# Performance work log

Measured on AMD Instinct MI355X. Metric: run time of the kernel, lower is better.

Reference implementation:

```python
import jax, jax.numpy as jnp
import numpy as np

V = 32000      # vocab_size
CTX = 1024     # context_length
D = 768        # n_embd
H = 12         # n_heads
HD = D // H    # head_dim
L = 6          # n_layers
DFF = 4 * D
B, S = 2, 1024
EPS = 1e-5


def _layernorm(x, w, b):
    mu = jnp.mean(x, axis=-1, keepdims=True)
    var = jnp.mean(jnp.square(x - mu), axis=-1, keepdims=True)
    return (x - mu) * jax.lax.rsqrt(var + EPS) * w + b


def setup_inputs() -> dict:
    key = jax.random.key(0)
    ks = iter(jax.random.split(key, 32))
    s = 0.02
    idx = jax.random.randint(next(ks), (B, S), 0, V)
    p = {
        "idx": idx,
        "tok_emb": jax.random.normal(next(ks), (V, D), jnp.float32) * s,
        "pos_emb": jax.random.normal(next(ks), (CTX, D), jnp.float32) * s,
        "ln1_w": jnp.ones((L, D)), "ln1_b": jnp.zeros((L, D)),
        "Wq": jax.random.normal(next(ks), (L, D, D), jnp.float32) * s,
        "bq": jnp.zeros((L, D)),
        "Wk": jax.random.normal(next(ks), (L, D, D), jnp.float32) * s,
        "bk": jnp.zeros((L, D)),
        "Wv": jax.random.normal(next(ks), (L, D, D), jnp.float32) * s,
        "bv": jnp.zeros((L, D)),
        "Wo": jax.random.normal(next(ks), (L, D, D), jnp.float32) * s,
        "bo": jnp.zeros((L, D)),
        "ln2_w": jnp.ones((L, D)), "ln2_b": jnp.zeros((L, D)),
        "W1": jax.random.normal(next(ks), (L, D, DFF), jnp.float32) * s,
        "b1": jnp.zeros((L, DFF)),
        "W2": jax.random.normal(next(ks), (L, DFF, D), jnp.float32) * s,
        "b2": jnp.zeros((L, D)),
        "lnf_w": jnp.ones((D,)), "lnf_b": jnp.zeros((D,)),
        "lm_head_w": jax.random.normal(next(ks), (D, V), jnp.float32) * s,
    }
    return p


def _forward(idx, tok_emb, pos_emb, ln1_w, ln1_b, Wq, bq, Wk, bk, Wv, bv,
             Wo, bo, ln2_w, ln2_b, W1, b1, W2, b2, lnf_w, lnf_b, lm_head_w):
    b, s = idx.shape
    x = tok_emb[idx] + pos_emb[:s]  # [B,S,D]
    mask = jnp.tril(jnp.ones((s, s), dtype=bool))  # causal
    scale = 1.0 / np.sqrt(HD)
    for l in range(L):
        # --- attention ---
        h = _layernorm(x, ln1_w[l], ln1_b[l])
        q = (h @ Wq[l] + bq[l]).reshape(b, s, H, HD).transpose(0, 2, 1, 3)
        k = (h @ Wk[l] + bk[l]).reshape(b, s, H, HD).transpose(0, 2, 1, 3)
        v = (h @ Wv[l] + bv[l]).reshape(b, s, H, HD).transpose(0, 2, 1, 3)
        att = jnp.einsum('bhqd,bhkd->bhqk', q, k) * scale
        att = jnp.where(mask, att, -jnp.inf)
        att = jax.nn.softmax(att, axis=-1)
        y = jnp.einsum('bhqk,bhkd->bhqd', att, v)
        y = y.transpose(0, 2, 1, 3).reshape(b, s, D)
        x = x + y @ Wo[l] + bo[l]
        # --- MLP ---
        h2 = _layernorm(x, ln2_w[l], ln2_b[l])
        x = x + jax.nn.relu(h2 @ W1[l] + b1[l]) @ W2[l] + b2[l]
    logits = _layernorm(x, lnf_w, lnf_b) @ lm_head_w  # [B,S,V]
    return logits


def reference(idx, tok_emb, pos_emb, ln1_w, ln1_b, Wq, bq, Wk, bk, Wv, bv,
              Wo, bo, ln2_w, ln2_b, W1, b1, W2, b2, lnf_w, lnf_b, lm_head_w):
    return _forward(idx, tok_emb, pos_emb, ln1_w, ln1_b, Wq, bq, Wk, bk, Wv,
                    bv, Wo, bo, ln2_w, ln2_b, W1, b1, W2, b2, lnf_w, lnf_b,
                    lm_head_w)
```

## Files before the change

### kernel.cpp

```cpp
#include <hip/hip_runtime.h>
#include <hip/hip_bf16.h>
#include <math.h>

#define D 768
#define NH 12
#define HD 64
#define NL 6
#define DFF 3072
#define BB 2
#define SS 1024
#define NROWS (BB*SS)
#define VOCAB 32000
#define QKVN (3*D)
#define LN_EPS 1e-5f

typedef __attribute__((ext_vector_type(8))) short bf16x8;
typedef __attribute__((ext_vector_type(4))) float f32x4;

typedef __attribute__((address_space(1))) const unsigned char* gas_ptr;
typedef __attribute__((address_space(3))) unsigned char* las_ptr;

__device__ __forceinline__ void load_lds16(const void* g, void* l) {
    __builtin_amdgcn_global_load_lds((gas_ptr)g, (las_ptr)l, 16, 0, 0);
}

__device__ __forceinline__ void storeOut(float* p, float v) { *p = v; }
__device__ __forceinline__ void storeOut(__hip_bfloat16* p, float v) { *p = __float2bfloat16(v); }
__device__ __forceinline__ ushort f2bs(float f) {
    __hip_bfloat16 h = __float2bfloat16(f);
    return *(ushort*)&h;
}

#define WAIT_VMCNT(n) asm volatile("s_waitcnt vmcnt(" #n ")" ::: "memory")

__global__ void embed_kernel(const int* __restrict__ idx, const float* __restrict__ tok,
                             const float* __restrict__ pos, float* __restrict__ x) {
    int row = blockIdx.x;
    int s = row % SS;
    int t = idx[row];
    for (int c = threadIdx.x; c < D; c += blockDim.x)
        x[row*D + c] = tok[(size_t)t*D + c] + pos[s*D + c];
}

template<typename OT>
__global__ __launch_bounds__(256) void layernorm_kernel(const float* __restrict__ x,
                                                        const float* __restrict__ w,
                                                        const float* __restrict__ b,
                                                        OT* __restrict__ out) {
    int row = blockIdx.x;
    __shared__ float l1[4], l2[4];
    int base = row * D;
    float vals[3];
    float s1 = 0.f, s2 = 0.f;
#pragma unroll
    for (int i = 0; i < 3; i++) {
        float v = x[base + threadIdx.x + i*256];
        vals[i] = v; s1 += v; s2 += v*v;
    }
#pragma unroll
    for (int o = 32; o > 0; o >>= 1) {
        s1 += __shfl_down(s1, o, 64);
        s2 += __shfl_down(s2, o, 64);
    }
    if ((threadIdx.x & 63) == 0) { l1[threadIdx.x >> 6] = s1; l2[threadIdx.x >> 6] = s2; }
    __syncthreads();
    float sum   = l1[0] + l1[1] + l1[2] + l1[3];
    float sumsq = l2[0] + l2[1] + l2[2] + l2[3];
    float mu  = sum * (1.f / D);
    float var = sumsq * (1.f / D) - mu * mu;
    float inv = rsqrtf(var + LN_EPS);
#pragma unroll
    for (int i = 0; i < 3; i++) {
        int c = threadIdx.x + i*256;
        storeOut(&out[base + c], (vals[i] - mu) * inv * w[c] + b[c]);
    }
}

__global__ __launch_bounds__(256) void transpose_cvt(const float* __restrict__ src,
                                                     __hip_bfloat16* __restrict__ dst,
                                                     int K, int N,
                                                     size_t srcLayerStride, size_t dstLayerStride,
                                                     int dstRowOff) {
    int l = blockIdx.z;
    src += (size_t)l * srcLayerStride;
    dst += (size_t)l * dstLayerStride + (size_t)dstRowOff * K;
    __shared__ float t[32][33];
    int k0 = blockIdx.x*32, n0 = blockIdx.y*32;
    int tx = threadIdx.x & 31, ty = threadIdx.x >> 5;
    for (int i = ty; i < 32; i += 8) t[i][tx] = src[(size_t)(k0+i)*N + n0+tx];
    __syncthreads();
    for (int i = ty; i < 32; i += 8) dst[(size_t)(n0+i)*K + k0+tx] = __float2bfloat16(t[tx][i]);
}

__global__ __launch_bounds__(256) void qkvo_trans(const float* __restrict__ Wq,
                                                  const float* __restrict__ Wk,
                                                  const float* __restrict__ Wv,
                                                  const float* __restrict__ Wo,
                                                  __hip_bfloat16* __restrict__ qkvT,
                                                  __hip_bfloat16* __restrict__ WoT) {
    int z = blockIdx.z, l = z >> 2, m = z & 3;
    const float* src = (m==0 ? Wq : m==1 ? Wk : m==2 ? Wv : Wo) + (size_t)l*D*D;
    __hip_bfloat16* dst = (m < 3) ? qkvT + (size_t)l*QKVN*D + (size_t)m*D*D
                                  : WoT  + (size_t)l*D*D;
    __shared__ float t[32][33];
    int k0 = blockIdx.x*32, n0 = blockIdx.y*32;
    int tx = threadIdx.x & 31, ty = threadIdx.x >> 5;
    for (int i = ty; i < 32; i += 8) t[i][tx] = src[(size_t)(k0+i)*D + n0+tx];
    __syncthreads();
    for (int i = ty; i < 32; i += 8) dst[(size_t)(n0+i)*D + k0+tx] = __float2bfloat16(t[tx][i]);
}

__global__ void pack_qkv_bias(const float* __restrict__ bq, const float* __restrict__ bk,
                              const float* __restrict__ bv, float* __restrict__ dst) {
    int l = blockIdx.y;
    int i = blockIdx.x*256 + threadIdx.x;
    dst[l*QKVN + i]         = bq[l*D + i];
    dst[l*QKVN + D + i]     = bk[l*D + i];
    dst[l*QKVN + 2*D + i]   = bv[l*D + i];
}

#define RG_STAGE(slot, k0) do {                                                  \
    _Pragma("unroll")                                                            \
    for (int i_ = 0; i_ < 2; i_++)                                               \
        load_lds16(A + (size_t)(bm + i_*64 + srow)*K + (k0) + sc_,               \
                   &AsR[slot][i_*64 + wid*16][0]);                               \
    load_lds16(BT + (size_t)(bn + srow)*K + (k0) + sc_,                          \
               &BsR[slot][wid*16][0]);                                           \
    } while (0)

template<typename OT, int RELU, int HASB, int VSTORE>
__global__ __launch_bounds__(256) void rg_gemm(const ushort* __restrict__ A,
                                               const ushort* __restrict__ BT,
                                               const float* __restrict__ bias,
                                               OT* __restrict__ C,
                                               ushort* __restrict__ vt,
                                               int N, int K, int gx) {
    constexpr int BM = 128, BN = 64;
    __shared__ ushort AsR[4][BM][32];
    __shared__ ushort BsR[4][BN][32];

    int id = blockIdx.x;
    int swz = (id & 7) * (gridDim.x >> 3) + (id >> 3);
    int by = swz / gx, bx = swz - by * gx;
    int bm = by * BM, bn = bx * BN;

    int tid = threadIdx.x;
    int lane = tid & 63, wid = tid >> 6;
    int wr = wid >> 1, wc = wid & 1;
    int srow = tid >> 2;
    int sc_ = ((tid & 3) ^ ((tid >> 3) & 3)) * 8;
    int fr = lane & 15, fc = lane >> 4;
    int rchunk = (fc ^ ((fr >> 1) & 3)) * 8;

    f32x4 acc[4][2];
#pragma unroll
    for (int i = 0; i < 4; i++)
#pragma unroll
        for (int j = 0; j < 2; j++)
#pragma unroll
            for (int r = 0; r < 4; r++) acc[i][j][r] = 0.f;

    const int NT = K / 32;
    RG_STAGE(0, 0);
    RG_STAGE(1, 32);
    RG_STAGE(2, 64);

    for (int t = 0; t < NT; t++) {
        int rem = NT - 1 - t;
        if (rem >= 2)      WAIT_VMCNT(6);
        else if (rem == 1) WAIT_VMCNT(3);
        else               WAIT_VMCNT(0);
        __builtin_amdgcn_s_barrier();
        asm volatile("" ::: "memory");
        if (t + 3 < NT) RG_STAGE((t+3) & 3, (t+3)*32);
        int s = t & 3;
        bf16x8 af[4], bf[2];
#pragma unroll
        for (int mi = 0; mi < 4; mi++)
            af[mi] = *(const bf16x8*)&AsR[s][wr*64 + mi*16 + fr][rchunk];
#pragma unroll
        for (int ni = 0; ni < 2; ni++)
            bf[ni] = *(const bf16x8*)&BsR[s][wc*32 + ni*16 + fr][rchunk];
        __builtin_amdgcn_s_setprio(1);
#pragma unroll
        for (int mi = 0; mi < 4; mi++)
#pragma unroll
            for (int ni = 0; ni < 2; ni++)
                acc[mi][ni] = __builtin_amdgcn_mfma_f32_16x16x32_bf16(af[mi], bf[ni], acc[mi][ni], 0, 0, 0);
        __builtin_amdgcn_s_setprio(0);
    }

    if (VSTORE && bn >= 2*D) {
        int hh = (bn - 2*D) / HD;
        int b  = bm >> 10;
        size_t vbase = ((size_t)(b*NH + hh)) * HD;
        int srow0 = (bm & (SS-1)) + wr*64 + fc*4;
#pragma unroll
        for (int mi = 0; mi < 4; mi++) {
#pragma unroll
            for (int ni = 0; ni < 2; ni++) {
                int col = bn + wc*32 + ni*16 + fr;
                int d   = wc*32 + ni*16 + fr;
                float bv_ = bias[col];
                ushort4 u;
                u.x = f2bs(acc[mi][ni][0] + bv_);
                u.y = f2bs(acc[mi][ni][1] + bv_);
                u.z = f2bs(acc[mi][ni][2] + bv_);
                u.w = f2bs(acc[mi][ni][3] + bv_);
                *(ushort4*)&vt[(vbase + d)*SS + srow0 + mi*16] = u;
            }
        }
    } else {
#pragma unroll
        for (int mi = 0; mi < 4; mi++) {
#pragma unroll
            for (int r = 0; r < 4; r++) {
                int row = bm + wr*64 + mi*16 + fc*4 + r;
#pragma unroll
                for (int ni = 0; ni < 2; ni++) {
                    int col = bn + wc*32 + ni*16 + fr;
                    float v = acc[mi][ni][r];
                    if (HASB) v += bias[col];
                    if (RELU) v = fmaxf(v, 0.f);
                    storeOut(&C[(size_t)row * N + col], v);
                }
            }
        }
    }
}

#define RSTAGE(slot, k0) do {                                                    \
    int row_ = tid >> 2;                                                         \
    load_lds16(A  + (size_t)(bm + row_)*K + (k0) + sc_,                          \
               (char*)As + (size_t)(slot)*4096 + (size_t)wid*1024);              \
    load_lds16(BT + (size_t)(bn + row_)*K + (k0) + sc_,                          \
               (char*)Bs + (size_t)(slot)*4096 + (size_t)wid*1024);              \
    } while (0)

template<int RELU>
__global__ __launch_bounds__(256) void gemm_ring64(const ushort* __restrict__ A,
                                                   const ushort* __restrict__ BT,
                                                   const float* __restrict__ bias,
                                                   const float* __restrict__ X,
                                                   float* __restrict__ C,
                                                   int N, int K, int gx) {
    __shared__ ushort As[6][64][32];
    __shared__ ushort Bs[6][64][32];

    int id = blockIdx.x;
    int swz = (id & 7) * (gridDim.x >> 3) + (id >> 3);
    int by = swz / gx, bx = swz - by * gx;
    int bm = by * 64, bn = bx * 64;

    int tid = threadIdx.x;
    int lane = tid & 63, wid = tid >> 6;
    int wr = wid >> 1, wc = wid & 1;
    int sc_ = ((lane & 3) ^ ((lane >> 3) & 3)) * 8;
    int fr = lane & 15, fc = lane >> 4;
    int rchunk = (fc ^ ((fr >> 1) & 3)) * 8;

    f32x4 acc[2][2];
#pragma unroll
    for (int i = 0; i < 2; i++)
#pragma unroll
        for (int j = 0; j < 2; j++)
#pragma unroll
            for (int r = 0; r < 4; r++) acc[i][j][r] = 0.f;

    const int NT = K / 32;
    RSTAGE(0, 0);
    RSTAGE(1, 32);
    RSTAGE(2, 64);
    RSTAGE(3, 96);
    RSTAGE(4, 128);

    for (int t = 0; t < NT; t++) {
        int rem = NT - t;
        if (rem >= 5)      WAIT_VMCNT(8);
        else if (rem == 4) WAIT_VMCNT(6);
        else if (rem == 3) WAIT_VMCNT(4);
        else if (rem == 2) WAIT_VMCNT(2);
        else               WAIT_VMCNT(0);
        __builtin_amdgcn_s_barrier();
        asm volatile("" ::: "memory");
        if (t + 5 < NT) RSTAGE((t+5) % 6, (t+5)*32);
        int s = t % 6;
        bf16x8 af[2], bf[2];
#pragma unroll
        for (int mi = 0; mi < 2; mi++)
            af[mi] = *(const bf16x8*)&As[s][wr*32 + mi*16 + fr][rchunk];
#pragma unroll
        for (int ni = 0; ni < 2; ni++)
            bf[ni] = *(const bf16x8*)&Bs[s][wc*32 + ni*16 + fr][rchunk];
        __builtin_amdgcn_s_setprio(1);
#pragma unroll
        for (int mi = 0; mi < 2; mi++)
#pragma unroll
            for (int ni = 0; ni < 2; ni++)
                acc[mi][ni] = __builtin_amdgcn_mfma_f32_16x16x32_bf16(af[mi], bf[ni], acc[mi][ni], 0, 0, 0);
        __builtin_amdgcn_s_setprio(0);
    }

#pragma unroll
    for (int mi = 0; mi < 2; mi++) {
#pragma unroll
        for (int r = 0; r < 4; r++) {
            int row = bm + wr*32 + mi*16 + fc*4 + r;
#pragma unroll
            for (int ni = 0; ni < 2; ni++) {
                int col = bn + wc*32 + ni*16 + fr;
                float v = acc[mi][ni][r] + bias[col] + X[(size_t)row * N + col];
                if (RELU) v = fmaxf(v, 0.f);
                C[(size_t)row * N + col] = v;
            }
        }
    }
}

#define LMSA3(slot, k0) do {                                                      \
    _Pragma("unroll")                                                             \
    for (int i_ = 0; i_ < 2; i_++) {                                              \
        int row_ = i_*128 + (tid >> 2);                                           \
        load_lds16(A + (size_t)(bm + row_)*D + (k0) + sc_,                        \
                   (char*)As3 + (size_t)(slot)*16384 + (size_t)(i_*512 + wid*64)*16); \
    } } while (0)
#define LMSB3(slot, k0) do {                                                      \
    _Pragma("unroll")                                                             \
    for (int i_ = 0; i_ < 2; i_++) {                                              \
        int row_ = i_*128 + (tid >> 2);                                           \
        load_lds16(BT + (size_t)(bm_n + row_)*D + (k0) + sc_,                     \
                   (char*)Bs3 + (size_t)(slot)*16384 + (size_t)(i_*512 + wid*64)*16); \
    } } while (0)

__global__ __launch_bounds__(512) void lm256_gemm(const ushort* __restrict__ A,
                                                  const ushort* __restrict__ BT,
                                                  float* __restrict__ C) {
    constexpr int NKT = D / 32;
    __shared__ ushort As3[3][256][32];
    __shared__ ushort Bs3[3][256][32];

    int id = blockIdx.x;
    int swz = (id & 7) * 125 + (id >> 3);
    int by = swz & 7;
    int bx = swz >> 3;
    int bm = by * 256, bm_n = bx * 256;

    int tid = threadIdx.x;
    int lane = tid & 63, wid = tid >> 6;
    int wr = wid >> 2, wc = wid & 3;
    int sc_ = ((tid & 3) ^ ((tid >> 3) & 3)) * 8;
    int fr = lane & 15, fc = lane >> 4;
    int rch = (fc ^ ((fr >> 1) & 3)) * 8;

    f32x4 acc[8][4];
#pragma unroll
    for (int i = 0; i < 8; i++)
#pragma unroll
        for (int j = 0; j < 4; j++)
#pragma unroll
            for (int r = 0; r < 4; r++) acc[i][j][r] = 0.f;

    LMSA3(0, 0);  LMSB3(0, 0);
    LMSA3(1, 32); LMSB3(1, 32);
    WAIT_VMCNT(4);
    __builtin_amdgcn_s_barrier();

    int s = 0;
    for (int j = 0; j < NKT; j++) {
        int s2 = s + 2; if (s2 >= 3) s2 -= 3;
        int kf2 = (j + 2) * 32;
        bf16x8 bfr[4], af[4];
#pragma unroll
        for (int ni = 0; ni < 4; ni++)
            bfr[ni] = *(const bf16x8*)&Bs3[s][wc*64 + ni*16 + fr][rch];
#pragma unroll
        for (int dm = 0; dm < 4; dm++)
            af[dm] = *(const bf16x8*)&As3[s][wr*128 + dm*16 + fr][rch];
        if (j + 2 < NKT) LMSA3(s2, kf2);
        __builtin_amdgcn_s_barrier();
        __builtin_amdgcn_s_setprio(1);
#pragma unroll
        for (int dm = 0; dm < 4; dm++)
#pragma unroll
            for (int ni = 0; ni < 4; ni++)
                acc[dm][ni] = __builtin_amdgcn_mfma_f32_16x16x32_bf16(af[dm], bfr[ni], acc[dm][ni], 0, 0, 0);
        __builtin_amdgcn_s_setprio(0);
        __builtin_amdgcn_s_barrier();
#pragma unroll
        for (int dm = 0; dm < 4; dm++)
            af[dm] = *(const bf16x8*)&As3[s][wr*128 + (4+dm)*16 + fr][rch];
        if (j + 2 < NKT) { LMSB3(s2, kf2); WAIT_VMCNT(2); }
        else             { WAIT_VMCNT(0); }
        __builtin_amdgcn_s_barrier();
        __builtin_amdgcn_s_setprio(1);
#pragma unroll
        for (int dm = 0; dm < 4; dm++)
#pragma unroll
            for (int ni = 0; ni < 4; ni++)
                acc[4+dm][ni] = __builtin_amdgcn_mfma_f32_16x16x32_bf16(af[dm], bfr[ni], acc[4+dm][ni], 0, 0, 0);
        __builtin_amdgcn_s_setprio(0);
        __builtin_amdgcn_s_barrier();
        s = s + 1; if (s >= 3) s = 0;
    }

#pragma unroll
    for (int mi = 0; mi < 8; mi++)
#pragma unroll
        for (int r = 0; r < 4; r++) {
            int row = bm + wr*128 + mi*16 + fc*4 + r;
            float* cp = C + (size_t)row * VOCAB + bm_n + wc*64 + fr;
#pragma unroll
            for (int ni = 0; ni < 4; ni++)
                cp[ni*16] = acc[mi][ni][r];
        }
}

#define KVSTAGE(buf, kv0) do {                                                   \
    _Pragma("unroll")                                                            \
    for (int j_ = 0; j_ < 2; j_++) {                                             \
        int r_ = w*16 + j_*8 + srow8;                                            \
        load_lds16(qkv + (size_t)(b*SS + (kv0) + r_)*QKVN + D + h*HD + schunk*8, \
                   &Ks[buf][w*16 + j_*8][0]);                                    \
        load_lds16(vt + ((size_t)(b*NH + h)*HD + r_)*SS + (kv0) + schunk*8,      \
                   &Vs[buf][w*16 + j_*8][0]);                                    \
    } } while (0)

__global__ __launch_bounds__(256) void attn_mfma(const ushort* __restrict__ qkv,
                                                 const ushort* __restrict__ vt,
                                                 __hip_bfloat16* __restrict__ y) {
    const int bx = blockIdx.x;
    const int qt = 15 - (bx & 15);
    const int h  = (bx >> 4) % NH;
    const int b  = bx / (16*NH);
    const int tid  = threadIdx.x;
    const int lane = tid & 63, w = tid >> 6;
    const int fr = lane & 15, fc = lane >> 4;

    __shared__ ushort Qs[64][64];
    __shared__ ushort Ks[3][64][64];
    __shared__ ushort Vs[3][64][64];
    __shared__ ushort Ps[4][16][72];

    const int q0 = qt * 64;
    const int srow8  = lane >> 3;
    const int schunk = (lane & 7) ^ srow8;

#pragma unroll
    for (int j = 0; j < 2; j++) {
        int r = w*16 + j*8 + srow8;
        load_lds16(qkv + (size_t)(b*SS + q0 + r)*QKVN + h*HD + schunk*8, &Qs[w*16 + j*8][0]);
    }
    KVSTAGE(0, 0);
    if (qt >= 1) { KVSTAGE(1, 64); WAIT_VMCNT(4); }
    else         { WAIT_VMCNT(0); }
    bf16x8 qf[2];
#pragma unroll
    for (int s_ = 0; s_ < 2; s_++)
        qf[s_] = *(const bf16x8*)&Qs[w*16 + fr][((s_*4 + fc) ^ (fr & 7))*8];

    f32x4 oacc[4];
#pragma unroll
    for (int ni = 0; ni < 4; ni++)
#pragma unroll
        for (int r = 0; r < 4; r++) oacc[ni][r] = 0.f;
    float m[4] = {-INFINITY, -INFINITY, -INFINITY, -INFINITY};
    float l[4] = {0.f, 0.f, 0.f, 0.f};

    int s = 0;
    for (int kt = 0; kt <= qt; kt++) {
        if (kt < qt) WAIT_VMCNT(4);
        else         WAIT_VMCNT(0);
        __builtin_amdgcn_s_barrier();
        asm volatile("" ::: "memory");
        if (kt + 2 <= qt) {
            int s2 = s + 2; if (s2 >= 3) s2 -= 3;
            KVSTAGE(s2, (kt+2)*64);
        }
        f32x4 sacc[4];
#pragma unroll
        for (int ni = 0; ni < 4; ni++)
#pragma unroll
            for (int r = 0; r < 4; r++) sacc[ni][r] = 0.f;
#pragma unroll
        for (int ni = 0; ni < 4; ni++)
#pragma unroll
            for (int s_ = 0; s_ < 2; s_++) {
                bf16x8 kf = *(const bf16x8*)&Ks[s][ni*16 + fr][((s_*4 + fc) ^ (fr & 7))*8];
                sacc[ni] = __builtin_amdgcn_mfma_f32_16x16x32_bf16(qf[s_], kf, sacc[ni], 0, 0, 0);
            }
        if (kt == qt) {
#pragma unroll
            for (int ni = 0; ni < 4; ni++)
#pragma unroll
                for (int r = 0; r < 4; r++) {
                    float v = sacc[ni][r] * 0.125f;
                    sacc[ni][r] = (ni*16 + fr > w*16 + fc*4 + r) ? -INFINITY : v;
                }
        } else {
#pragma unroll
            for (int ni = 0; ni < 4; ni++)
#pragma unroll
                for (int r = 0; r < 4; r++) sacc[ni][r] *= 0.125f;
        }
        float p[4][4];
#pragma unroll
        for (int r = 0; r < 4; r++) {
            float mx = fmaxf(fmaxf(sacc[0][r], sacc[1][r]), fmaxf(sacc[2][r], sacc[3][r]));
#pragma unroll
            for (int o = 1; o < 16; o <<= 1) mx = fmaxf(mx, __shfl_xor(mx, o, 64));
            float mn = fmaxf(m[r], mx);
            float fac = __expf(m[r] - mn);
            float rs = 0.f;
#pragma unroll
            for (int ni = 0; ni < 4; ni++) {
                float pv = __expf(sacc[ni][r] - mn);
                p[ni][r] = pv;
                rs += pv;
            }
#pragma unroll
            for (int o = 1; o < 16; o <<= 1) rs += __shfl_xor(rs, o, 64);
            l[r] = l[r] * fac + rs;
            m[r] = mn;
#pragma unroll
            for (int ni = 0; ni < 4; ni++) oacc[ni][r] *= fac;
        }
#pragma unroll
        for (int ni = 0; ni < 4; ni++)
#pragma unroll
            for (int r = 0; r < 4; r++)
                Ps[w][fc*4 + r][ni*16 + fr] = f2bs(p[ni][r]);
        bf16x8 pa[2];
#pragma unroll
        for (int s_ = 0; s_ < 2; s_++) pa[s_] = *(const bf16x8*)&Ps[w][fr][s_*32 + fc*8];
#pragma unroll
        for (int ni = 0; ni < 4; ni++)
#pragma unroll
            for (int s_ = 0; s_ < 2; s_++) {
                bf16x8 vf = *(const bf16x8*)&Vs[s][ni*16 + fr][((s_*4 + fc) ^ (fr & 7))*8];
                oacc[ni] = __builtin_amdgcn_mfma_f32_16x16x32_bf16(pa[s_], vf, oacc[ni], 0, 0, 0);
            }
        s = s + 1; if (s >= 3) s = 0;
    }
#pragma unroll
    for (int r = 0; r < 4; r++) {
        float rinv = 1.f / l[r];
        int row = b*SS + q0 + w*16 + fc*4 + r;
#pragma unroll
        for (int ni = 0; ni < 4; ni++)
            y[(size_t)row*D + h*HD + ni*16 + fr] = __float2bfloat16(oacc[ni][r] * rinv);
    }
}

extern "C" void kernel_launch(void* const* d_in, const int* in_sizes, int n_in,
                              void* d_out, int out_size, void* d_ws, size_t ws_size,
                              hipStream_t stream) {
    const int*   idx  = (const int*)d_in[0];
    const float* tok  = (const float*)d_in[1];
    const float* pos  = (const float*)d_in[2];
    const float* ln1w = (const float*)d_in[3];
    const float* ln1b = (const float*)d_in[4];
    const float* Wq   = (const float*)d_in[5];
    const float* bq   = (const float*)d_in[6];
    const float* Wk   = (const float*)d_in[7];
    const float* bk   = (const float*)d_in[8];
    const float* Wv   = (const float*)d_in[9];
    const float* bv   = (const float*)d_in[10];
    const float* Wo   = (const float*)d_in[11];
    const float* bo   = (const float*)d_in[12];
    const float* ln2w = (const float*)d_in[13];
    const float* ln2b = (const float*)d_in[14];
    const float* W1   = (const float*)d_in[15];
    const float* b1   = (const float*)d_in[16];
    const float* W2   = (const float*)d_in[17];
    const float* b2   = (const float*)d_in[18];
    const float* lnfw = (const float*)d_in[19];
    const float* lnfb = (const float*)d_in[20];
    const float* lmw  = (const float*)d_in[21];
    float* out = (float*)d_out;

    char* p = (char*)d_ws;
    __hip_bfloat16* qkvT = (__hip_bfloat16*)p; p += (size_t)NL*QKVN*D*2;
    __hip_bfloat16* WoT  = (__hip_bfloat16*)p; p += (size_t)NL*D*D*2;
    __hip_bfloat16* W1T  = (__hip_bfloat16*)p; p += (size_t)NL*DFF*D*2;
    __hip_bfloat16* W2T  = (__hip_bfloat16*)p; p += (size_t)NL*D*DFF*2;
    __hip_bfloat16* lmT  = (__hip_bfloat16*)p; p += (size_t)VOCAB*D*2;
    float*          bqkv = (float*)p;          p += (size_t)NL*QKVN*4;
    float*          x    = (float*)p;          p += (size_t)NROWS*D*4;
    __hip_bfloat16* h    = (__hip_bfloat16*)p; p += (size_t)NROWS*D*2;
    __hip_bfloat16* qkv  = (__hip_bfloat16*)p; p += (size_t)NROWS*QKVN*2;
    __hip_bfloat16* vt   = (__hip_bfloat16*)p; p += (size_t)BB*NH*HD*SS*2;
    __hip_bfloat16* yb   = (__hip_bfloat16*)p; p += (size_t)NROWS*D*2;
    __hip_bfloat16* a1   = (__hip_bfloat16*)p; p += (size_t)NROWS*DFF*2;

    qkvo_trans<<<dim3(D/32, D/32, NL*4), 256, 0, stream>>>(Wq, Wk, Wv, Wo, qkvT, WoT);
    transpose_cvt<<<dim3(D/32, DFF/32, NL), 256, 0, stream>>>(W1, W1T, D, DFF, (size_t)D*DFF, (size_t)DFF*D, 0);
    transpose_cvt<<<dim3(DFF/32, D/32, NL), 256, 0, stream>>>(W2, W2T, DFF, D, (size_t)DFF*D, (size_t)D*DFF, 0);
    transpose_cvt<<<dim3(D/32, VOCAB/32, 1), 256, 0, stream>>>(lmw, lmT, D, VOCAB, 0, 0, 0);
    pack_qkv_bias<<<dim3(3, NL), 256, 0, stream>>>(bq, bk, bv, bqkv);

    embed_kernel<<<NROWS, 256, 0, stream>>>(idx, tok, pos, x);

    for (int l = 0; l < NL; l++) {
        layernorm_kernel<<<NROWS, 256, 0, stream>>>(x, ln1w + l*D, ln1b + l*D, h);
        rg_gemm<__hip_bfloat16,0,1,1><<<576, 256, 0, stream>>>(
            (const ushort*)h, (const ushort*)(qkvT + (size_t)l*QKVN*D),
            bqkv + (size_t)l*QKVN, qkv, (ushort*)vt, QKVN, D, QKVN/64);
        attn_mfma<<<BB*NH*(SS/64), 256, 0, stream>>>((const ushort*)qkv, (const ushort*)vt, yb);
        gemm_ring64<0><<<384, 256, 0, stream>>>(
            (const ushort*)yb, (const ushort*)(WoT + (size_t)l*D*D),
            bo + (size_t)l*D, x, x, D, D, D/64);
        layernorm_kernel<<<NROWS, 256, 0, stream>>>(x, ln2w + l*D, ln2b + l*D, h);
        rg_gemm<__hip_bfloat16,1,1,0><<<768, 256, 0, stream>>>(
            (const ushort*)h, (const ushort*)(W1T + (size_t)l*DFF*D),
            b1 + (size_t)l*DFF, a1, nullptr, DFF, D, DFF/64);
        gemm_ring64<0><<<384, 256, 0, stream>>>(
            (const ushort*)a1, (const ushort*)(W2T + (size_t)l*D*DFF),
            b2 + (size_t)l*D, x, x, D, DFF, D/64);
    }
    layernorm_kernel<<<NROWS, 256, 0, stream>>>(x, lnfw, lnfb, h);
    lm256_gemm<<<1000, 512, 0, stream>>>((const ushort*)h, (const ushort*)lmT, out);
}
```

Baseline: 1.191 ms.

## Fold LayerNorm into following GEMMs via weight scaling and epilogue correction

Removes the standalone LayerNorm kernels by folding gamma into the transposed bf16 weights and precomputing column sums (gamma·W and beta·W + bias). Each GEMM computes per-row mean and rstd from its bf16 input tile in a prologue and applies them in the epilogue. The residual stream x is also switched from fp32 to bf16, halving its traffic, at some risk to accuracy accumulated across layers. The cost is redundant row-stat recomputation in every column block and extra setup kernels for the column sums.

```diff
diff --git a/kernel.cpp b/kernel.cpp
--- a/kernel.cpp
+++ b/kernel.cpp
@@ -24,78 +24,49 @@
     __builtin_amdgcn_global_load_lds((gas_ptr)g, (las_ptr)l, 16, 0, 0);
 }
 
-__device__ __forceinline__ void storeOut(float* p, float v) { *p = v; }
-__device__ __forceinline__ void storeOut(__hip_bfloat16* p, float v) { *p = __float2bfloat16(v); }
 __device__ __forceinline__ ushort f2bs(float f) {
     __hip_bfloat16 h = __float2bfloat16(f);
     return *(ushort*)&h;
 }
+__device__ __forceinline__ float bs2f(ushort u) {
+    unsigned v = ((unsigned)u) << 16;
+    float f; __builtin_memcpy(&f, &v, 4); return f;
+}
 
 #define WAIT_VMCNT(n) asm volatile("s_waitcnt vmcnt(" #n ")" ::: "memory")
 
 __global__ void embed_kernel(const int* __restrict__ idx, const float* __restrict__ tok,
-                             const float* __restrict__ pos, float* __restrict__ x) {
+                             const float* __restrict__ pos, __hip_bfloat16* __restrict__ x) {
     int row = blockIdx.x;
     int s = row % SS;
     int t = idx[row];
     for (int c = threadIdx.x; c < D; c += blockDim.x)
-        x[row*D + c] = tok[(size_t)t*D + c] + pos[s*D + c];
-}
-
-template<typename OT>
-__global__ __launch_bounds__(256) void layernorm_kernel(const float* __restrict__ x,
-                                                        const float* __restrict__ w,
-                                                        const float* __restrict__ b,
-                                                        OT* __restrict__ out) {
-    int row = blockIdx.x;
-    __shared__ float l1[4], l2[4];
-    int base = row * D;
-    float vals[3];
-    float s1 = 0.f, s2 = 0.f;
-#pragma unroll
-    for (int i = 0; i < 3; i++) {
-        float v = x[base + threadIdx.x + i*256];
-        vals[i] = v; s1 += v; s2 += v*v;
-    }
-#pragma unroll
-    for (int o = 32; o > 0; o >>= 1) {
-        s1 += __shfl_down(s1, o, 64);
-        s2 += __shfl_down(s2, o, 64);
-    }
-    if ((threadIdx.x & 63) == 0) { l1[threadIdx.x >> 6] = s1; l2[threadIdx.x >> 6] = s2; }
-    __syncthreads();
-    float sum   = l1[0] + l1[1] + l1[2] + l1[3];
-    float sumsq = l2[0] + l2[1] + l2[2] + l2[3];
-    float mu  = sum * (1.f / D);
-    float var = sumsq * (1.f / D) - mu * mu;
-    float inv = rsqrtf(var + LN_EPS);
-#pragma unroll
-    for (int i = 0; i < 3; i++) {
-        int c = threadIdx.x + i*256;
-        storeOut(&out[base + c], (vals[i] - mu) * inv * w[c] + b[c]);
-    }
+        x[row*D + c] = __float2bfloat16(tok[(size_t)t*D + c] + pos[s*D + c]);
 }
 
 __global__ __launch_bounds__(256) void transpose_cvt(const float* __restrict__ src,
                                                      __hip_bfloat16* __restrict__ dst,
                                                      int K, int N,
-                                                     size_t srcLayerStride, size_t dstLayerStride,
-                                                     int dstRowOff) {
+                                                     size_t srcLs, size_t dstLs,
+                                                     const float* __restrict__ foldw, size_t fLs) {
     int l = blockIdx.z;
-    src += (size_t)l * srcLayerStride;
-    dst += (size_t)l * dstLayerStride + (size_t)dstRowOff * K;
+    src += (size_t)l * srcLs;
+    dst += (size_t)l * dstLs;
     __shared__ float t[32][33];
     int k0 = blockIdx.x*32, n0 = blockIdx.y*32;
     int tx = threadIdx.x & 31, ty = threadIdx.x >> 5;
     for (int i = ty; i < 32; i += 8) t[i][tx] = src[(size_t)(k0+i)*N + n0+tx];
     __syncthreads();
-    for (int i = ty; i < 32; i += 8) dst[(size_t)(n0+i)*K + k0+tx] = __float2bfloat16(t[tx][i]);
+    float fac = foldw ? foldw[l*fLs + k0 + tx] : 1.f;
+    for (int i = ty; i < 32; i += 8)
+        dst[(size_t)(n0+i)*K + k0+tx] = __float2bfloat16(t[tx][i] * fac);
 }
 
 __global__ __launch_bounds__(256) void qkvo_trans(const float* __restrict__ Wq,
                                                   const float* __restrict__ Wk,
                                                   const float* __restrict__ Wv,
                                                   const float* __restrict__ Wo,
+                                                  const float* __restrict__ ln1w,
                                                   __hip_bfloat16* __restrict__ qkvT,
                                                   __hip_bfloat16* __restrict__ WoT) {
     int z = blockIdx.z, l = z >> 2, m = z & 3;
@@ -107,16 +78,48 @@
     int tx = threadIdx.x & 31, ty = threadIdx.x >> 5;
     for (int i = ty; i < 32; i += 8) t[i][tx] = src[(size_t)(k0+i)*D + n0+tx];
     __syncthreads();
-    for (int i = ty; i < 32; i += 8) dst[(size_t)(n0+i)*D + k0+tx] = __float2bfloat16(t[tx][i]);
-}
-
-__global__ void pack_qkv_bias(const float* __restrict__ bq, const float* __restrict__ bk,
-                              const float* __restrict__ bv, float* __restrict__ dst) {
+    float fac = (m < 3) ? ln1w[l*D + k0 + tx] : 1.f;
+    for (int i = ty; i < 32; i += 8)
+        dst[(size_t)(n0+i)*D + k0+tx] = __float2bfloat16(t[tx][i] * fac);
+}
+
+__global__ void colsum_qkv(const float* __restrict__ Wq, const float* __restrict__ Wk,
+                           const float* __restrict__ Wv,
+                           const float* __restrict__ ln1w, const float* __restrict__ ln1b,
+                           const float* __restrict__ bq, const float* __restrict__ bk,
+                           const float* __restrict__ bv,
+                           float* __restrict__ outW, float* __restrict__ outC) {
+    int l = blockIdx.y, m = blockIdx.z;
+    int n = blockIdx.x*256 + threadIdx.x;
+    const float* W    = (m==0 ? Wq : m==1 ? Wk : Wv) + (size_t)l*D*D;
+    const float* bias = (m==0 ? bq : m==1 ? bk : bv) + (size_t)l*D;
+    const float* w = ln1w + (size_t)l*D;
+    const float* b = ln1b + (size_t)l*D;
+    float sW = 0.f, sC = 0.f;
+    for (int k = 0; k < D; k++) {
+        float Wk_ = W[(size_t)k*D + n];
+        sW += w[k]*Wk_; sC += b[k]*Wk_;
+    }
+    outW[(size_t)l*QKVN + m*D + n] = sW;
+    outC[(size_t)l*QKVN + m*D + n] = sC + bias[n];
+}
+
+__global__ void colsum_gen(const float* __restrict__ W, const float* __restrict__ w,
+                           const float* __restrict__ b, const float* __restrict__ bias,
+                           float* __restrict__ outW, float* __restrict__ outC,
+                           int K, int N, size_t wLs, size_t vLs, size_t oLs) {
     int l = blockIdx.y;
-    int i = blockIdx.x*256 + threadIdx.x;
-    dst[l*QKVN + i]         = bq[l*D + i];
-    dst[l*QKVN + D + i]     = bk[l*D + i];
-    dst[l*QKVN + 2*D + i]   = bv[l*D + i];
+    int n = blockIdx.x*256 + threadIdx.x;
+    const float* Wp = W + (size_t)l*wLs;
+    const float* wp = w + (size_t)l*vLs;
+    const float* bp = b + (size_t)l*vLs;
+    float sW = 0.f, sC = 0.f;
+    for (int k = 0; k < K; k++) {
+        float Wk_ = Wp[(size_t)k*N + n];
+        sW += wp[k]*Wk_; sC += bp[k]*Wk_;
+    }
+    outW[(size_t)l*oLs + n] = sW;
+    outC[(size_t)l*oLs + n] = sC + (bias ? bias[(size_t)l*oLs + n] : 0.f);
 }
 
 #define RG_STAGE(slot, k0) do {                                                  \
@@ -128,16 +131,18 @@
                &BsR[slot][wid*16][0]);                                           \
     } while (0)
 
-template<typename OT, int RELU, int HASB, int VSTORE>
+template<int RELU, int VSTORE>
 __global__ __launch_bounds__(256) void rg_gemm(const ushort* __restrict__ A,
                                                const ushort* __restrict__ BT,
-                                               const float* __restrict__ bias,
-                                               OT* __restrict__ C,
+                                               const float* __restrict__ wW,
+                                               const float* __restrict__ bc,
+                                               __hip_bfloat16* __restrict__ C,
                                                ushort* __restrict__ vt,
                                                int N, int K, int gx) {
     constexpr int BM = 128, BN = 64;
     __shared__ ushort AsR[4][BM][32];
     __shared__ ushort BsR[4][BN][32];
+    __shared__ float muinv[128][2];
 
     int id = blockIdx.x;
     int swz = (id & 7) * (gridDim.x >> 3) + (id >> 3);
@@ -151,6 +156,29 @@
     int sc_ = ((tid & 3) ^ ((tid >> 3) & 3)) * 8;
     int fr = lane & 15, fc = lane >> 4;
     int rchunk = (fc ^ ((fr >> 1) & 3)) * 8;
+
+    {
+        int row = tid >> 1, half = tid & 1;
+        const ushort* xr = A + (size_t)(bm + row)*K + half*(K >> 1);
+        float s1 = 0.f, s2 = 0.f;
+        for (int i = 0; i < K/16; i++) {
+            bf16x8 v = *(const bf16x8*)(xr + i*8);
+#pragma unroll
+            for (int j = 0; j < 8; j++) {
+                float f = bs2f((ushort)v[j]);
+                s1 += f; s2 += f*f;
+            }
+        }
+        s1 += __shfl_xor(s1, 1, 64);
+        s2 += __shfl_xor(s2, 1, 64);
+        if (half == 0) {
+            float mu  = s1 * (1.f / D);
+            float var = s2 * (1.f / D) - mu*mu;
+            muinv[row][0] = mu;
+            muinv[row][1] = rsqrtf(var + LN_EPS);
+        }
+    }
+    __syncthreads();
 
     f32x4 acc[4][2];
 #pragma unroll
@@ -199,14 +227,17 @@
         for (int mi = 0; mi < 4; mi++) {
 #pragma unroll
             for (int ni = 0; ni < 2; ni++) {
-                int col = bn + wc*32 + ni*16 + fr;
                 int d   = wc*32 + ni*16 + fr;
-                float bv_ = bias[col];
+                int col = bn + d;
+                float wWc = wW[col], bcc = bc[col];
                 ushort4 u;
-                u.x = f2bs(acc[mi][ni][0] + bv_);
-                u.y = f2bs(acc[mi][ni][1] + bv_);
-                u.z = f2bs(acc[mi][ni][2] + bv_);
-                u.w = f2bs(acc[mi][ni][3] + bv_);
+#pragma unroll
+                for (int r = 0; r < 4; r++) {
+                    int rl = wr*64 + mi*16 + fc*4 + r;
+                    float mu = muinv[rl][0], inv = muinv[rl][1];
+                    float v = acc[mi][ni][r]*inv - mu*inv*wWc + bcc;
+                    ((ushort*)&u)[r] = f2bs(v);
+                }
                 *(ushort4*)&vt[(vbase + d)*SS + srow0 + mi*16] = u;
             }
         }
@@ -215,14 +246,15 @@
         for (int mi = 0; mi < 4; mi++) {
 #pragma unroll
             for (int r = 0; r < 4; r++) {
-                int row = bm + wr*64 + mi*16 + fc*4 + r;
+                int rl = wr*64 + mi*16 + fc*4 + r;
+                float mu = muinv[rl][0], inv = muinv[rl][1];
+                int row = bm + rl;
 #pragma unroll
                 for (int ni = 0; ni < 2; ni++) {
                     int col = bn + wc*32 + ni*16 + fr;
-                    float v = acc[mi][ni][r];
-                    if (HASB) v += bias[col];
+                    float v = acc[mi][ni][r]*inv - mu*inv*wW[col] + bc[col];
                     if (RELU) v = fmaxf(v, 0.f);
-                    storeOut(&C[(size_t)row * N + col], v);
+                    C[(size_t)row * N + col] = __float2bfloat16(v);
                 }
             }
         }
@@ -237,12 +269,11 @@
                (char*)Bs + (size_t)(slot)*4096 + (size_t)wid*1024);              \
     } while (0)
 
-template<int RELU>
 __global__ __launch_bounds__(256) void gemm_ring64(const ushort* __restrict__ A,
                                                    const ushort* __restrict__ BT,
                                                    const float* __restrict__ bias,
-                                                   const float* __restrict__ X,
-                                                   float* __restrict__ C,
+                                                   const __hip_bfloat16* __restrict__ X,
+                                                   __hip_bfloat16* __restrict__ C,
                                                    int N, int K, int gx) {
     __shared__ ushort As[6][64][32];
     __shared__ ushort Bs[6][64][32];
@@ -309,9 +340,8 @@
 #pragma unroll
             for (int ni = 0; ni < 2; ni++) {
                 int col = bn + wc*32 + ni*16 + fr;
-                float v = acc[mi][ni][r] + bias[col] + X[(size_t)row * N + col];
-                if (RELU) v = fmaxf(v, 0.f);
-                C[(size_t)row * N + col] = v;
+                float v = acc[mi][ni][r] + bias[col] + __bfloat162float(X[(size_t)row * N + col]);
+                C[(size_t)row * N + col] = __float2bfloat16(v);
             }
         }
     }
@@ -334,10 +364,13 @@
 
 __global__ __launch_bounds__(512) void lm256_gemm(const ushort* __restrict__ A,
                                                   const ushort* __restrict__ BT,
+                                                  const float* __restrict__ wW,
+                                                  const float* __restrict__ bc,
                                                   float* __restrict__ C) {
     constexpr int NKT = D / 32;
     __shared__ ushort As3[3][256][32];
     __shared__ ushort Bs3[3][256][32];
+    __shared__ float muinvL[256][2];
 
     int id = blockIdx.x;
     int swz = (id & 7) * 125 + (id >> 3);
@@ -352,6 +385,29 @@
     int fr = lane & 15, fc = lane >> 4;
     int rch = (fc ^ ((fr >> 1) & 3)) * 8;
 
+    {
+        int row = tid >> 1, half = tid & 1;
+        const ushort* xr = A + (size_t)(bm + row)*D + half*(D >> 1);
+        float s1 = 0.f, s2 = 0.f;
+        for (int i = 0; i < D/16; i++) {
+            bf16x8 v = *(const bf16x8*)(xr + i*8);
+#pragma unroll
+            for (int j = 0; j < 8; j++) {
+                float f = bs2f((ushort)v[j]);
+                s1 += f; s2 += f*f;
+            }
+        }
+        s1 += __shfl_xor(s1, 1, 64);
+        s2 += __shfl_xor(s2, 1, 64);
+        if (half == 0) {
+            float mu  = s1 * (1.f / D);
+            float var = s2 * (1.f / D) - mu*mu;
+            muinvL[row][0] = mu;
+            muinvL[row][1] = rsqrtf(var + LN_EPS);
+        }
+    }
+    __syncthreads();
+
     f32x4 acc[8][4];
 #pragma unroll
     for (int i = 0; i < 8; i++)
@@ -367,7 +423,7 @@
 
     int s = 0;
     for (int j = 0; j < NKT; j++) {
-        int s2 = s + 2; if (s2 >= 3) s2 -= 3;
+        int s2_ = s + 2; if (s2_ >= 3) s2_ -= 3;
         int kf2 = (j + 2) * 32;
         bf16x8 bfr[4], af[4];
 #pragma unroll
@@ -376,7 +432,7 @@
 #pragma unroll
         for (int dm = 0; dm < 4; dm++)
             af[dm] = *(const bf16x8*)&As3[s][wr*128 + dm*16 + fr][rch];
-        if (j + 2 < NKT) LMSA3(s2, kf2);
+        if (j + 2 < NKT) LMSA3(s2_, kf2);
         __builtin_amdgcn_s_barrier();
         __builtin_amdgcn_s_setprio(1);
 #pragma unroll
@@ -389,7 +445,7 @@
 #pragma unroll
         for (int dm = 0; dm < 4; dm++)
             af[dm] = *(const bf16x8*)&As3[s][wr*128 + (4+dm)*16 + fr][rch];
-        if (j + 2 < NKT) { LMSB3(s2, kf2); WAIT_VMCNT(2); }
+        if (j + 2 < NKT) { LMSB3(s2_, kf2); WAIT_VMCNT(2); }
         else             { WAIT_VMCNT(0); }
         __builtin_amdgcn_s_barrier();
         __builtin_amdgcn_s_setprio(1);
@@ -407,11 +463,15 @@
     for (int mi = 0; mi < 8; mi++)
 #pragma unroll
         for (int r = 0; r < 4; r++) {
-            int row = bm + wr*128 + mi*16 + fc*4 + r;
+            int rl = wr*128 + mi*16 + fc*4 + r;
+            float mu = muinvL[rl][0], inv = muinvL[rl][1];
+            int row = bm + rl;
             float* cp = C + (size_t)row * VOCAB + bm_n + wc*64 + fr;
 #pragma unroll
-            for (int ni = 0; ni < 4; ni++)
-                cp[ni*16] = acc[mi][ni][r];
+            for (int ni = 0; ni < 4; ni++) {
+                int col = bm_n + wc*64 + ni*16 + fr;
+                cp[ni*16] = acc[mi][ni][r]*inv - mu*inv*wW[col] + bc[col];
+            }
         }
 }
 
@@ -584,39 +644,45 @@
     __hip_bfloat16* W1T  = (__hip_bfloat16*)p; p += (size_t)NL*DFF*D*2;
     __hip_bfloat16* W2T  = (__hip_bfloat16*)p; p += (size_t)NL*D*DFF*2;
     __hip_bfloat16* lmT  = (__hip_bfloat16*)p; p += (size_t)VOCAB*D*2;
-    float*          bqkv = (float*)p;          p += (size_t)NL*QKVN*4;
-    float*          x    = (float*)p;          p += (size_t)NROWS*D*4;
-    __hip_bfloat16* h    = (__hip_bfloat16*)p; p += (size_t)NROWS*D*2;
+    float* qkv_wW = (float*)p;                 p += (size_t)NL*QKVN*4;
+    float* qkv_bc = (float*)p;                 p += (size_t)NL*QKVN*4;
+    float* w1_wW  = (float*)p;                 p += (size_t)NL*DFF*4;
+    float* w1_bc  = (float*)p;                 p += (size_t)NL*DFF*4;
+    float* lm_wW  = (float*)p;                 p += (size_t)VOCAB*4;
+    float* lm_bc  = (float*)p;                 p += (size_t)VOCAB*4;
+    __hip_bfloat16* x    = (__hip_bfloat16*)p; p += (size_t)NROWS*D*2;
     __hip_bfloat16* qkv  = (__hip_bfloat16*)p; p += (size_t)NROWS*QKVN*2;
     __hip_bfloat16* vt   = (__hip_bfloat16*)p; p += (size_t)BB*NH*HD*SS*2;
     __hip_bfloat16* yb   = (__hip_bfloat16*)p; p += (size_t)NROWS*D*2;
     __hip_bfloat16* a1   = (__hip_bfloat16*)p; p += (size_t)NROWS*DFF*2;
 
-    qkvo_trans<<<dim3(D/32, D/32, NL*4), 256, 0, stream>>>(Wq, Wk, Wv, Wo, qkvT, WoT);
-    transpose_cvt<<<dim3(D/32, DFF/32, NL), 256, 0, stream>>>(W1, W1T, D, DFF, (size_t)D*DFF, (size_t)DFF*D, 0);
-    transpose_cvt<<<dim3(DFF/32, D/32, NL), 256, 0, stream>>>(W2, W2T, DFF, D, (size_t)DFF*D, (size_t)D*DFF, 0);
-    transpose_cvt<<<dim3(D/32, VOCAB/32, 1), 256, 0, stream>>>(lmw, lmT, D, VOCAB, 0, 0, 0);
-    pack_qkv_bias<<<dim3(3, NL), 256, 0, stream>>>(bq, bk, bv, bqkv);
-
+    qkvo_trans<<<dim3(D/32, D/32, NL*4), 256, 0, stream>>>(Wq, Wk, Wv, Wo, ln1w, qkvT, WoT);
+    transpose_cvt<<<dim3(D/32, DFF/32, NL), 256, 0, stream>>>(W1, W1T, D, DFF, (size_t)D*DFF, (size_t)DFF*D, ln2w, D);
+    transpose_cvt<<<dim3(DFF/32, D/32, NL), 256, 0, stream>>>(W2, W2T, DFF, D, (size_t)DFF*D, (size_t)D*DFF, nullptr, 0);
+    transpose_cvt<<<dim3(D/32, VOCAB/32, 1), 256, 0, stream>>>(lmw, lmT, D, VOCAB, 0, 0, lnfw, 0);
+    colsum_qkv<<<dim3(3, NL, 3), 256, 0, stream>>>(Wq, Wk, Wv, ln1w, ln1b, bq, bk, bv, qkv_wW, qkv_bc);
+    colsum_gen<<<dim3(DFF/256, NL), 256, 0, stream>>>(W1, ln2w, ln2b, b1, w1_wW, w1_bc,
+                                                      D, DFF, (size_t)D*DFF, D, DFF);
+    colsum_gen<<<dim3(VOCAB/256, 1), 256, 0, stream>>>(lmw, lnfw, lnfb, nullptr, lm_wW, lm_bc,
+                                                       D, VOCAB, 0, 0, 0);
     embed_kernel<<<NROWS, 256, 0, stream>>>(idx, tok, pos, x);
 
     for (int l = 0; l < NL; l++) {
-        layernorm_kernel<<<NROWS, 256, 0, stream>>>(x, ln1w + l*D, ln1b + l*D, h);
-        rg_gemm<__hip_bfloat16,0,1,1><<<576, 256, 0, stream>>>(
-            (const ushort*)h, (const ushort*)(qkvT + (size_t)l*QKVN*D),
-            bqkv + (size_t)l*QKVN, qkv, (ushort*)vt, QKVN, D, QKVN/64);
+        rg_gemm<0,1><<<576, 256, 0, stream>>>(
+            (const ushort*)x, (const ushort*)(qkvT + (size_t)l*QKVN*D),
+            qkv_wW + (size_t)l*QKVN, qkv_bc + (size_t)l*QKVN,
+            qkv, (ushort*)vt, QKVN, D, QKVN/64);
         attn_mfma<<<BB*NH*(SS/64), 256, 0, stream>>>((const ushort*)qkv, (const ushort*)vt, yb);
-        gemm_ring64<0><<<384, 256, 0, stream>>>(
+        gemm_ring64<<<384, 256, 0, stream>>>(
             (const ushort*)yb, (const ushort*)(WoT + (size_t)l*D*D),
             bo + (size_t)l*D, x, x, D, D, D/64);
-        layernorm_kernel<<<NROWS, 256, 0, stream>>>(x, ln2w + l*D, ln2b + l*D, h);
-        rg_gemm<__hip_bfloat16,1,1,0><<<768, 256, 0, stream>>>(
-            (const ushort*)h, (const ushort*)(W1T + (size_t)l*DFF*D),
-            b1 + (size_t)l*DFF, a1, nullptr, DFF, D, DFF/64);
-        gemm_ring64<0><<<384, 256, 0, stream>>>(
+        rg_gemm<1,0><<<768, 256, 0, stream>>>(
+            (const ushort*)x, (const ushort*)(W1T + (size_t)l*DFF*D),
+            w1_wW + (size_t)l*DFF, w1_bc + (size_t)l*DFF,
+            a1, nullptr, DFF, D, DFF/64);
+        gemm_ring64<<<384, 256, 0, stream>>>(
             (const ushort*)a1, (const ushort*)(W2T + (size_t)l*D*DFF),
             b2 + (size_t)l*D, x, x, D, DFF, D/64);
     }
-    layernorm_kernel<<<NROWS, 256, 0, stream>>>(x, lnfw, lnfb, h);
-    lm256_gemm<<<1000, 512, 0, stream>>>((const ushort*)h, (const ushort*)lmT, out);
-}
+    lm256_gemm<<<1000, 512, 0, stream>>>((const ushort*)x, (const ushort*)lmT, lm_wW, lm_bc, out);
+}
```

New measurement: 2.183 ms. +83.3%, slower.

## Use 128x128-tile triple-buffered MFMA GEMM for the MLP up-projection

Applied to the files above, without the earlier changes.

Adds a new g128_gemm kernel with 128x128 output tiles per block, each wave computing 64x64, and a three-slot LDS ring filled by direct global-to-LDS loads. It also splits loads and MFMA work into two half-phases with barriers and priority hints. It replaces the rg_gemm launch for the W1 GEMM plus bias plus ReLU, halving the block count to 384. The goal is more operand reuse per LDS load and better overlap of loads with compute. The cost is more registers and LDS per block and fewer blocks to fill the CUs.

```diff
diff --git a/kernel.cpp b/kernel.cpp
--- a/kernel.cpp
+++ b/kernel.cpp
@@ -224,6 +224,108 @@
                     if (RELU) v = fmaxf(v, 0.f);
                     storeOut(&C[(size_t)row * N + col], v);
                 }
+            }
+        }
+    }
+}
+
+#define G128A(slot, k0) do {                                                     \
+    _Pragma("unroll")                                                            \
+    for (int i_ = 0; i_ < 2; i_++)                                               \
+        load_lds16(A + (size_t)(bm + i_*64 + (tid >> 2))*K + (k0) + sc_,         \
+                   &GA[slot][i_*64 + wid*16][0]);                                \
+    } while (0)
+#define G128B(slot, k0) do {                                                     \
+    _Pragma("unroll")                                                            \
+    for (int i_ = 0; i_ < 2; i_++)                                               \
+        load_lds16(BT + (size_t)(bn + i_*64 + (tid >> 2))*K + (k0) + sc_,        \
+                   &GB[slot][i_*64 + wid*16][0]);                                \
+    } while (0)
+
+template<int RELU>
+__global__ __launch_bounds__(256) void g128_gemm(const ushort* __restrict__ A,
+                                                 const ushort* __restrict__ BT,
+                                                 const float* __restrict__ bias,
+                                                 __hip_bfloat16* __restrict__ C,
+                                                 int N, int K, int gx) {
+    __shared__ ushort GA[3][128][32];
+    __shared__ ushort GB[3][128][32];
+
+    int id = blockIdx.x;
+    int swz = (id & 7) * (gridDim.x >> 3) + (id >> 3);
+    int by = swz / gx, bx = swz - by * gx;
+    int bm = by * 128, bn = bx * 128;
+
+    int tid = threadIdx.x;
+    int lane = tid & 63, wid = tid >> 6;
+    int wr = wid >> 1, wc = wid & 1;
+    int sc_ = ((tid & 3) ^ ((tid >> 3) & 3)) * 8;
+    int fr = lane & 15, fc = lane >> 4;
+    int rch = (fc ^ ((fr >> 1) & 3)) * 8;
+
+    f32x4 acc[4][4];
+#pragma unroll
+    for (int i = 0; i < 4; i++)
+#pragma unroll
+        for (int j = 0; j < 4; j++)
+#pragma unroll
+            for (int r = 0; r < 4; r++) acc[i][j][r] = 0.f;
+
+    const int NT = K / 32;
+    G128A(0, 0);  G128B(0, 0);
+    G128A(1, 32); G128B(1, 32);
+    WAIT_VMCNT(4);
+    __builtin_amdgcn_s_barrier();
+
+    int s = 0;
+    for (int j = 0; j < NT; j++) {
+        int s2 = s + 2; if (s2 >= 3) s2 -= 3;
+        int kf2 = (j + 2) * 32;
+        bf16x8 bfr[4], af[2];
+#pragma unroll
+        for (int ni = 0; ni < 4; ni++)
+            bfr[ni] = *(const bf16x8*)&GB[s][wc*64 + ni*16 + fr][rch];
+#pragma unroll
+        for (int mi = 0; mi < 2; mi++)
+            af[mi] = *(const bf16x8*)&GA[s][wr*64 + mi*16 + fr][rch];
+        if (j + 2 < NT) G128A(s2, kf2);
+        __builtin_amdgcn_s_barrier();
+        __builtin_amdgcn_s_setprio(1);
+#pragma unroll
+        for (int mi = 0; mi < 2; mi++)
+#pragma unroll
+            for (int ni = 0; ni < 4; ni++)
+                acc[mi][ni] = __builtin_amdgcn_mfma_f32_16x16x32_bf16(af[mi], bfr[ni], acc[mi][ni], 0, 0, 0);
+        __builtin_amdgcn_s_setprio(0);
+        __builtin_amdgcn_s_barrier();
+#pragma unroll
+        for (int mi = 0; mi < 2; mi++)
+            af[mi] = *(const bf16x8*)&GA[s][wr*64 + (2+mi)*16 + fr][rch];
+        if (j + 2 < NT) { G128B(s2, kf2); WAIT_VMCNT(4); }
+        else             { WAIT_VMCNT(0); }
+        __builtin_amdgcn_s_barrier();
+        __builtin_amdgcn_s_setprio(1);
+#pragma unroll
+        for (int mi = 0; mi < 2; mi++)
+#pragma unroll
+            for (int ni = 0; ni < 4; ni++)
+                acc[2+mi][ni] = __builtin_amdgcn_mfma_f32_16x16x32_bf16(af[mi], bfr[ni], acc[2+mi][ni], 0, 0, 0);
+        __builtin_amdgcn_s_setprio(0);
+        __builtin_amdgcn_s_barrier();
+        s = s + 1; if (s >= 3) s = 0;
+    }
+
+#pragma unroll
+    for (int mi = 0; mi < 4; mi++) {
+#pragma unroll
+        for (int r = 0; r < 4; r++) {
+            int row = bm + wr*64 + mi*16 + fc*4 + r;
+#pragma unroll
+            for (int ni = 0; ni < 4; ni++) {
+                int col = bn + wc*64 + ni*16 + fr;
+                float v = acc[mi][ni][r] + bias[col];
+                if (RELU) v = fmaxf(v, 0.f);
+                C[(size_t)row * N + col] = __float2bfloat16(v);
             }
         }
     }
@@ -610,9 +712,9 @@
             (const ushort*)yb, (const ushort*)(WoT + (size_t)l*D*D),
             bo + (size_t)l*D, x, x, D, D, D/64);
         layernorm_kernel<<<NROWS, 256, 0, stream>>>(x, ln2w + l*D, ln2b + l*D, h);
-        rg_gemm<__hip_bfloat16,1,1,0><<<768, 256, 0, stream>>>(
+        g128_gemm<1><<<384, 256, 0, stream>>>(
             (const ushort*)h, (const ushort*)(W1T + (size_t)l*DFF*D),
-            b1 + (size_t)l*DFF, a1, nullptr, DFF, D, DFF/64);
+            b1 + (size_t)l*DFF, a1, DFF, D, DFF/128);
         gemm_ring64<0><<<384, 256, 0, stream>>>(
             (const ushort*)a1, (const ushort*)(W2T + (size_t)l*D*DFF),
             b2 + (size_t)l*D, x, x, D, DFF, D/64);
```

New measurement: 1.194 ms. Within noise of the previous version (+0.3%).
